# Kernel optimization log

Measured on AMD Instinct MI355X. Metric: run time of the kernel, lower is better.

The kernel has to match this reference:

```python
import jax, jax.numpy as jnp
import numpy as np

BS, N, D_IN, D_OUT = 4, 512, 64, 64
TEMP = 1.0
POOL_K = 0.5
N_KEEP = max(int(N * POOL_K), 1)  # 256
BN_EPS = 1e-5


def setup_inputs() -> dict:
    key = jax.random.key(0)
    ks = jax.random.split(key, 12)
    xav = lambda k, shape: jax.random.normal(k, shape, jnp.float32) * np.sqrt(2.0 / sum(shape))
    return {
        "x": jax.random.normal(ks[0], (BS, N, D_IN), jnp.float32),
        "att_proj_w": xav(ks[1], (D_IN, D_OUT)),
        "att_proj_b": jnp.zeros((D_OUT,), jnp.float32),
        "att_weight": xav(ks[2], (D_OUT, 1))[:, 0],  # (D_OUT,)
        "pwa_w": xav(ks[3], (D_IN, D_OUT)),
        "pwa_b": jnp.zeros((D_OUT,), jnp.float32),
        "pwoa_w": xav(ks[4], (D_IN, D_OUT)),
        "pwoa_b": jnp.zeros((D_OUT,), jnp.float32),
        "bn_gamma": jnp.ones((D_OUT,), jnp.float32),
        "bn_beta": jnp.zeros((D_OUT,), jnp.float32),
        "bn_mean": jnp.zeros((D_OUT,), jnp.float32),
        "bn_var": jnp.ones((D_OUT,), jnp.float32),
        "pool_w": xav(ks[5], (D_OUT, 1))[:, 0],  # (D_OUT,)
        "pool_b": jnp.zeros((), jnp.float32),
    }


def reference(x, att_proj_w, att_proj_b, att_weight, pwa_w, pwa_b,
              pwoa_w, pwoa_b, bn_gamma, bn_beta, bn_mean, bn_var,
              pool_w, pool_b):
    # ---- GraphAttentionLayer (eval mode: dropout off, BN uses running stats) ----
    # pairwise node product: (bs, i, j, d)
    pair = x[:, :, None, :] * x[:, None, :, :]
    a = jnp.tanh(jnp.einsum('bijd,de->bije', pair, att_proj_w) + att_proj_b)
    scores = jnp.einsum('bije,e->bij', a, att_weight) / TEMP
    att = jax.nn.softmax(scores, axis=-1)  # torch softmax over dim=-2 of (bs,i,j,1) == j axis
    agg = jnp.einsum('bij,bjd->bid', att, x)
    h = (agg @ pwa_w + pwa_b) + (x @ pwoa_w + pwoa_b)
    h = (h - bn_mean) * jax.lax.rsqrt(bn_var + BN_EPS) * bn_gamma + bn_beta
    h = jax.nn.selu(h)
    # ---- GraphPool (eval: dropout off) ----
    s = jax.nn.sigmoid(h @ pool_w + pool_b)  # (bs, N)
    _, idx = jax.lax.top_k(s, N_KEEP)        # (bs, N_KEEP), sorted desc like torch.topk
    hs = h * s[..., None]
    out = jnp.take_along_axis(hs, idx[..., None], axis=1)  # (bs, N_KEEP, D_OUT)
    return out
```

## Files before the change

### kernel.cpp

```cpp
#include <hip/hip_runtime.h>
#include <hip/hip_bf16.h>
#include <math.h>

#define BSZ 4
#define NN 512
#define DD 64
#define NKEEP 256

typedef __attribute__((ext_vector_type(8))) short short8;
typedef __attribute__((ext_vector_type(4))) float f32x4;

__device__ __forceinline__ ushort f2bf_rne(float f) {
  union { float f; unsigned u; } v; v.f = f;
  unsigned r = v.u + 0x7fffu + ((v.u >> 16) & 1u);
  return (ushort)(r >> 16);
}
__device__ __forceinline__ float bf2f(ushort h) {
  union { unsigned u; float f; } v; v.u = ((unsigned)h) << 16;
  return v.f;
}

__global__ __launch_bounds__(256, 2) void k_score(
    const float* __restrict__ x, const float* __restrict__ apw,
    const float* __restrict__ apb, const float* __restrict__ aw,
    float* __restrict__ sTp) {
  __shared__ ushort Yh[2][4 * 16 * 64];
  __shared__ ushort Yl[2][4 * 16 * 64];

  const int t = threadIdx.x;
  const int w = t >> 6, l = t & 63;
  const int bid = blockIdx.x;
  const int b = bid / 288;
  const int rem = bid % 288;
  const int eh = rem / 144;
  const int tid = rem % 144;
  int m, base;
  if (tid < 40) {
    if (tid < 4)        { m = 0; base = 0; }
    else if (tid < 12)  { m = 1; base = 4; }
    else if (tid < 24)  { m = 2; base = 12; }
    else                { m = 3; base = 24; }
  } else {
    if (tid < 60)       { m = 4; base = 40; }
    else if (tid < 84)  { m = 5; base = 60; }
    else if (tid < 112) { m = 6; base = 84; }
    else                { m = 7; base = 112; }
  }
  const int it = tid - base;
  const int i0 = it * 16;
  const int jb0 = m * 64;
  const int eh32 = eh * 32;
  const bool fast = (jb0 >= i0 + 16);

  const float* xb = x + (size_t)b * NN * DD;
  const int j0 = jb0 + w * 16;
  const bool wave_active = (j0 + 16 > i0);

  short8 ah[2], al[2];
  if (wave_active) {
    const int g = l >> 4;
    const int j = j0 + (l & 15);
    #pragma unroll
    for (int ks = 0; ks < 2; ++ks) {
      const float* xr = xb + (size_t)j * DD + ks * 32 + g * 8;
      float4 u0 = *reinterpret_cast<const float4*>(xr);
      float4 u1 = *reinterpret_cast<const float4*>(xr + 4);
      float vv[8] = {u0.x, u0.y, u0.z, u0.w, u1.x, u1.y, u1.z, u1.w};
      short8 hh, ll;
      #pragma unroll
      for (int qq = 0; qq < 8; ++qq) {
        ushort hq = f2bf_rne(vv[qq]);
        hh[qq] = (short)hq;
        ll[qq] = (short)f2bf_rne(vv[qq] - bf2f(hq));
      }
      ah[ks] = hh; al[ks] = ll;
    }
  }

  float awC = 0.f;
  #pragma unroll 8
  for (int e = 0; e < 32; ++e) awC += aw[eh32 + e];

  const int bi_g = l >> 4;
  const int bdq = (l & 15) * 4;
  auto build = [&](int rnd, int bf) {
    const int e = eh32 + rnd * 4 + w;
    float wt[4];
    #pragma unroll
    for (int k = 0; k < 4; ++k) wt[k] = apw[(bdq + k) * 64 + e];
    #pragma unroll
    for (int i2 = 0; i2 < 4; ++i2) {
      const int i = i2 * 4 + bi_g;
      float4 xv = *reinterpret_cast<const float4*>(
          xb + (size_t)(i0 + i) * DD + bdq);
      const float p0v = xv.x * wt[0], p1v = xv.y * wt[1];
      const float p2v = xv.z * wt[2], p3v = xv.w * wt[3];
      const ushort h0 = f2bf_rne(p0v), h1 = f2bf_rne(p1v);
      const ushort h2 = f2bf_rne(p2v), h3 = f2bf_rne(p3v);
      uint2 hw, lw;
      hw.x = (uint)h0 | ((uint)h1 << 16);
      hw.y = (uint)h2 | ((uint)h3 << 16);
      lw.x = (uint)f2bf_rne(p0v - bf2f(h0)) | ((uint)f2bf_rne(p1v - bf2f(h1)) << 16);
      lw.y = (uint)f2bf_rne(p2v - bf2f(h2)) | ((uint)f2bf_rne(p3v - bf2f(h3)) << 16);
      const int byteoff = (w * 2048 + (i * 64 + bdq) * 2) ^ ((i & 7) << 4);
      *reinterpret_cast<uint2*>(reinterpret_cast<char*>(Yh[bf]) + byteoff) = hw;
      *reinterpret_cast<uint2*>(reinterpret_cast<char*>(Yl[bf]) + byteoff) = lw;
    }
  };

  const int il = l & 15, g = l >> 4;
  const int fbyte0 = ((il * 64 + g * 8) * 2) ^ ((il & 7) << 4);
  const int fbyte1 = ((il * 64 + 32 + g * 8) * 2) ^ ((il & 7) << 4);
  const float K2 = 2.8853900817779268f;

  f32x4 srews = (f32x4){0.f, 0.f, 0.f, 0.f};

  build(0, 0);

  #pragma unroll 1
  for (int r = 0; r < 8; ++r) {
    __syncthreads();
    const char* Ph = reinterpret_cast<const char*>(Yh[r & 1]);
    const char* Pl = reinterpret_cast<const char*>(Yl[r & 1]);

    short8 cbh0, cbh1, cbl0, cbl1;
    if (wave_active) {
      cbh0 = *reinterpret_cast<const short8*>(Ph + fbyte0);
      cbh1 = *reinterpret_cast<const short8*>(Ph + fbyte1);
      cbl0 = *reinterpret_cast<const short8*>(Pl + fbyte0);
      cbl1 = *reinterpret_cast<const short8*>(Pl + fbyte1);
    }
    if (r < 7) build(r + 1, (r + 1) & 1);

    if (wave_active) {
      #pragma unroll
      for (int p = 0; p < 4; ++p) {
        short8 nbh0, nbh1, nbl0, nbl1;
        if (p < 3) {
          nbh0 = *reinterpret_cast<const short8*>(Ph + (p + 1) * 2048 + fbyte0);
          nbh1 = *reinterpret_cast<const short8*>(Ph + (p + 1) * 2048 + fbyte1);
          nbl0 = *reinterpret_cast<const short8*>(Pl + (p + 1) * 2048 + fbyte0);
          nbl1 = *reinterpret_cast<const short8*>(Pl + (p + 1) * 2048 + fbyte1);
        }
        f32x4 a0 = (f32x4){0.f, 0.f, 0.f, 0.f};
        f32x4 a1 = (f32x4){0.f, 0.f, 0.f, 0.f};
        a0 = __builtin_amdgcn_mfma_f32_16x16x32_bf16(ah[0], cbh0, a0, 0, 0, 0);
        a1 = __builtin_amdgcn_mfma_f32_16x16x32_bf16(ah[1], cbh1, a1, 0, 0, 0);
        a0 = __builtin_amdgcn_mfma_f32_16x16x32_bf16(ah[0], cbl0, a0, 0, 0, 0);
        a1 = __builtin_amdgcn_mfma_f32_16x16x32_bf16(ah[1], cbl1, a1, 0, 0, 0);
        a0 = __builtin_amdgcn_mfma_f32_16x16x32_bf16(al[0], cbh0, a0, 0, 0, 0);
        a1 = __builtin_amdgcn_mfma_f32_16x16x32_bf16(al[1], cbh1, a1, 0, 0, 0);

        const int e = eh32 + r * 4 + p;
        const float bias = apb[e];
        const float aw2 = 2.f * aw[e];
        #pragma unroll
        for (int rr = 0; rr < 4; ++rr) {
          const float vv = a0[rr] + a1[rr] + bias;
          const float ex = __builtin_amdgcn_exp2f(vv * K2);
          const float rc = __builtin_amdgcn_rcpf(ex + 1.0f);
          srews[rr] = fmaf(-aw2, rc, srews[rr]);
        }
        cbh0 = nbh0; cbh1 = nbh1; cbl0 = nbl0; cbl1 = nbl1;
      }
    }
  }

  f32x4 sv4;
  #pragma unroll
  for (int rr = 0; rr < 4; ++rr) sv4[rr] = srews[rr] + awC;

  float* plane = sTp + ((size_t)(eh * 4 + b)) * NN * NN;
  const int iv = i0 + il;
  if (fast) {
    #pragma unroll
    for (int rr = 0; rr < 4; ++rr)
      plane[(size_t)(j0 + g * 4 + rr) * NN + iv] = sv4[rr];
    __syncthreads();
    float* T = reinterpret_cast<float*>(Yh[0]);
    {
      const int byteoff = ((il * 64 + w * 16 + g * 4) * 4) ^ ((il & 7) << 4);
      *reinterpret_cast<f32x4*>(reinterpret_cast<char*>(T) + byteoff) = sv4;
    }
    __syncthreads();
    {
      const int row = t >> 4, cb4 = (t & 15) * 4;
      const int byteoff = ((row * 64 + cb4) * 4) ^ ((row & 7) << 4);
      f32x4 v = *reinterpret_cast<const f32x4*>(
          reinterpret_cast<const char*>(T) + byteoff);
      *reinterpret_cast<f32x4*>(plane + (size_t)(i0 + row) * NN + jb0 + cb4) = v;
    }
  } else if (wave_active) {
    #pragma unroll
    for (int rr = 0; rr < 4; ++rr) {
      const int jv = j0 + g * 4 + rr;
      if (jv >= iv) plane[(size_t)iv * NN + jv] = sv4[rr];
      if (jv > iv) plane[(size_t)jv * NN + iv] = sv4[rr];
    }
  }
}

__global__ __launch_bounds__(256) void k_soft(
    const float* __restrict__ x, const float* __restrict__ sTp,
    const float* __restrict__ pwa, const float* __restrict__ pwab,
    const float* __restrict__ pwoa, const float* __restrict__ pwob,
    const float* __restrict__ gam, const float* __restrict__ bet,
    const float* __restrict__ mu, const float* __restrict__ var,
    const float* __restrict__ poolw, const float* __restrict__ poolb,
    float* __restrict__ h, float* __restrict__ s) {
  __shared__ float ssc[2][512];
  __shared__ float srm[2][4], srs[2][4];
  __shared__ float sagg[4][2][64];
  __shared__ float rag[2][64], xis[2][64];

  const int t = threadIdx.x;
  const int w = t >> 6, l = t & 63;
  const int b = blockIdx.x >> 8;
  const int rp = blockIdx.x & 255;
  const int i_r0 = rp * 2, i_r1 = i_r0 + 1;
  const float* xb = x + (size_t)b * NN * DD;
  const float* pl0 = sTp + (size_t)b * NN * NN;
  const float* pl1 = sTp + (size_t)(4 + b) * NN * NN;
  const int jw = w * 128;

  const size_t o0 = (size_t)i_r0 * NN + jw + l;
  const size_t o1 = (size_t)i_r1 * NN + jw + l;
  float r0a = pl0[o0] + pl1[o0];
  float r0b = pl0[o0 + 64] + pl1[o0 + 64];
  float r1a = pl0[o1] + pl1[o1];
  float r1b = pl0[o1 + 64] + pl1[o1 + 64];
  float m0 = fmaxf(r0a, r0b), m1 = fmaxf(r1a, r1b);
  #pragma unroll
  for (int off = 32; off; off >>= 1) {
    m0 = fmaxf(m0, __shfl_xor(m0, off, 64));
    m1 = fmaxf(m1, __shfl_xor(m1, off, 64));
  }
  if (l == 0) { srm[0][w] = m0; srm[1][w] = m1; }
  __syncthreads();
  m0 = fmaxf(fmaxf(srm[0][0], srm[0][1]), fmaxf(srm[0][2], srm[0][3]));
  m1 = fmaxf(fmaxf(srm[1][0], srm[1][1]), fmaxf(srm[1][2], srm[1][3]));

  const float L2E = 1.4426950408889634f;
  float e0a = __builtin_amdgcn_exp2f((r0a - m0) * L2E);
  float e0b = __builtin_amdgcn_exp2f((r0b - m0) * L2E);
  float e1a = __builtin_amdgcn_exp2f((r1a - m1) * L2E);
  float e1b = __builtin_amdgcn_exp2f((r1b - m1) * L2E);
  float ps0 = e0a + e0b, ps1 = e1a + e1b;
  #pragma unroll
  for (int off = 32; off; off >>= 1) {
    ps0 += __shfl_xor(ps0, off, 64);
    ps1 += __shfl_xor(ps1, off, 64);
  }
  if (l == 0) { srs[0][w] = ps0; srs[1][w] = ps1; }
  __syncthreads();
  const float inv0 = 1.f / (srs[0][0] + srs[0][1] + srs[0][2] + srs[0][3]);
  const float inv1 = 1.f / (srs[1][0] + srs[1][1] + srs[1][2] + srs[1][3]);
  ssc[0][jw + l] = e0a * inv0;
  ssc[0][jw + 64 + l] = e0b * inv0;
  ssc[1][jw + l] = e1a * inv1;
  ssc[1][jw + 64 + l] = e1b * inv1;
  __syncthreads();

  float g0a = 0.f, g0b = 0.f, g1a = 0.f, g1b = 0.f;
  #pragma unroll 4
  for (int jj = 0; jj < 128; jj += 2) {
    const int j = jw + jj;
    const float xv0 = xb[(size_t)j * DD + l];
    const float xv1 = xb[(size_t)(j + 1) * DD + l];
    g0a = fmaf(ssc[0][j], xv0, g0a);
    g1a = fmaf(ssc[1][j], xv0, g1a);
    g0b = fmaf(ssc[0][j + 1], xv1, g0b);
    g1b = fmaf(ssc[1][j + 1], xv1, g1b);
  }
  sagg[w][0][l] = g0a + g0b;
  sagg[w][1][l] = g1a + g1b;
  __syncthreads();

  if (w < 2) {
    const int irow = i_r0 + w;
    rag[w][l] = sagg[0][w][l] + sagg[1][w][l] + sagg[2][w][l] + sagg[3][w][l];
    xis[w][l] = xb[(size_t)irow * DD + l];
    float acc = 0.f;
    #pragma unroll 8
    for (int d = 0; d < 64; ++d) {
      acc = fmaf(rag[w][d], pwa[d * 64 + l], acc);
      acc = fmaf(xis[w][d], pwoa[d * 64 + l], acc);
    }
    acc += pwab[l] + pwob[l];
    float hb = (acc - mu[l]) * rsqrtf(var[l] + 1e-5f) * gam[l] + bet[l];
    const float SC = 1.0507009873554805f, AL = 1.6732632423543772f;
    float hv = hb > 0.f ? SC * hb : SC * AL * expm1f(hb);
    h[((size_t)(b * NN + irow)) * DD + l] = hv;

    float p = hv * poolw[l];
    #pragma unroll
    for (int off = 32; off; off >>= 1) p += __shfl_xor(p, off, 64);
    if (l == 0) s[b * NN + irow] = 1.f / (1.f + expf(-(p + poolb[0])));
  }
}

__global__ __launch_bounds__(512) void k_sel(
    const float* __restrict__ s, const float* __restrict__ h,
    float* __restrict__ out) {
  __shared__ float svv[NN];
  __shared__ int inv[NKEEP];
  __shared__ float sval[NKEEP];
  const int b = blockIdx.x, t = threadIdx.x;
  svv[t] = s[b * NN + t];
  __syncthreads();

  const float my = svv[t];
  int r = 0;
  #pragma unroll 4
  for (int j0 = 0; j0 < NN; j0 += 4) {
    float4 v = *reinterpret_cast<const float4*>(&svv[j0]);
    r += (v.x > my) || (v.x == my && (j0 + 0) < t);
    r += (v.y > my) || (v.y == my && (j0 + 1) < t);
    r += (v.z > my) || (v.z == my && (j0 + 2) < t);
    r += (v.w > my) || (v.w == my && (j0 + 3) < t);
  }
  if (r < NKEEP) { inv[r] = t; sval[r] = my; }
  __syncthreads();

  #pragma unroll
  for (int pos = t; pos < NKEEP * 16; pos += 512) {
    const int kk = pos >> 4, d4 = (pos & 15) * 4;
    const int i = inv[kk];
    const float sc = sval[kk];
    float4 v = *reinterpret_cast<const float4*>(
        h + ((size_t)(b * NN + i)) * DD + d4);
    v.x *= sc; v.y *= sc; v.z *= sc; v.w *= sc;
    *reinterpret_cast<float4*>(out + ((size_t)(b * NKEEP + kk)) * DD + d4) = v;
  }
}

extern "C" void kernel_launch(void* const* d_in, const int* in_sizes, int n_in,
                              void* d_out, int out_size, void* d_ws, size_t ws_size,
                              hipStream_t stream) {
  const float* x     = (const float*)d_in[0];
  const float* apw   = (const float*)d_in[1];
  const float* apb   = (const float*)d_in[2];
  const float* aw    = (const float*)d_in[3];
  const float* pwa   = (const float*)d_in[4];
  const float* pwab  = (const float*)d_in[5];
  const float* pwoa  = (const float*)d_in[6];
  const float* pwob  = (const float*)d_in[7];
  const float* gam   = (const float*)d_in[8];
  const float* bet   = (const float*)d_in[9];
  const float* mu    = (const float*)d_in[10];
  const float* var   = (const float*)d_in[11];
  const float* poolw = (const float*)d_in[12];
  const float* poolb = (const float*)d_in[13];
  float* out = (float*)d_out;

  float* sTp = (float*)d_ws;
  float* h   = sTp + (size_t)2 * BSZ * NN * NN;
  float* s   = h + (size_t)BSZ * NN * DD;

  k_score<<<1152, 256, 0, stream>>>(x, apw, apb, aw, sTp);
  k_soft<<<BSZ * 256, 256, 0, stream>>>(x, sTp, pwa, pwab, pwoa, pwob,
                                        gam, bet, mu, var, poolw, poolb, h, s);
  k_sel<<<BSZ, 512, 0, stream>>>(s, h, out);
}
```

Measured before the change: 71.26 us.

## Restructure score kernel: pair-product A operand, pre-split weights, single score plane

The score kernel now forms the elementwise pair product x_i*x_j as the MFMA A operand and multiplies by a pre-split (hi/lo bf16) transposed weight matrix held in registers, covering all 64 output features per block. The previous version used a two-half-plane layout that k_soft had to sum. A new prep kernel builds the split weights and a triangular tile table, and k_score runs as 64-thread single-wave blocks over 16x16 upper-triangle tiles. Each tile writes its transposed mirror through a small shared tile. This drops the per-round shared-memory staging and syncs, and halves the score-plane traffic. In exchange it adds an extra kernel launch, more MFMAs per output element, and per-row cross-lane shuffle reductions.

```diff
diff --git a/kernel.cpp b/kernel.cpp
--- a/kernel.cpp
+++ b/kernel.cpp
@@ -19,189 +19,171 @@
   union { unsigned u; float f; } v; v.u = ((unsigned)h) << 16;
   return v.f;
 }
-
-__global__ __launch_bounds__(256, 2) void k_score(
-    const float* __restrict__ x, const float* __restrict__ apw,
-    const float* __restrict__ apb, const float* __restrict__ aw,
-    float* __restrict__ sTp) {
-  __shared__ ushort Yh[2][4 * 16 * 64];
-  __shared__ ushort Yl[2][4 * 16 * 64];
-
-  const int t = threadIdx.x;
-  const int w = t >> 6, l = t & 63;
-  const int bid = blockIdx.x;
-  const int b = bid / 288;
-  const int rem = bid % 288;
-  const int eh = rem / 144;
-  const int tid = rem % 144;
-  int m, base;
-  if (tid < 40) {
-    if (tid < 4)        { m = 0; base = 0; }
-    else if (tid < 12)  { m = 1; base = 4; }
-    else if (tid < 24)  { m = 2; base = 12; }
-    else                { m = 3; base = 24; }
-  } else {
-    if (tid < 60)       { m = 4; base = 40; }
-    else if (tid < 84)  { m = 5; base = 60; }
-    else if (tid < 112) { m = 6; base = 84; }
-    else                { m = 7; base = 112; }
-  }
-  const int it = tid - base;
-  const int i0 = it * 16;
-  const int jb0 = m * 64;
-  const int eh32 = eh * 32;
-  const bool fast = (jb0 >= i0 + 16);
+__device__ __forceinline__ void split2(float a, float b, uint& hu, uint& lu) {
+  const ushort ha = f2bf_rne(a), hb = f2bf_rne(b);
+  hu = (uint)ha | ((uint)hb << 16);
+  const ushort la = f2bf_rne(a - bf2f(ha));
+  const ushort lb = f2bf_rne(b - bf2f(hb));
+  lu = (uint)la | ((uint)lb << 16);
+}
+
+__global__ void k_prep(const float* __restrict__ apw,
+                       ushort* __restrict__ wht, ushort* __restrict__ wlt,
+                       int* __restrict__ tile_tab) {
+  const int idx = blockIdx.x * 256 + threadIdx.x;
+  const int d = idx >> 6, e = idx & 63;
+  const float wv = apw[idx];
+  const ushort h = f2bf_rne(wv);
+  const ushort lo = f2bf_rne(wv - bf2f(h));
+  wht[e * 64 + d] = h;
+  wlt[e * 64 + d] = lo;
+  if (idx < 528) {
+    int it = 0;
+    #pragma unroll
+    for (int r = 1; r < 32; ++r) it += ((r * (65 - r)) / 2 <= idx);
+    const int jt = it + (idx - (it * (65 - it)) / 2);
+    tile_tab[idx] = it | (jt << 8);
+  }
+}
+
+__global__ __launch_bounds__(64) void k_score(
+    const float* __restrict__ x, const ushort* __restrict__ wht,
+    const ushort* __restrict__ wlt, const float* __restrict__ apb,
+    const float* __restrict__ aw, const int* __restrict__ tile_tab,
+    float* __restrict__ sT) {
+  __shared__ __align__(16) float T[16][16];
+
+  const int l = threadIdx.x;
+  const int il = l & 15, g = l >> 4;
+  const int gid = blockIdx.x;
+  const int b = gid / 528;
+  const int pid = gid - b * 528;
+  const int pk = tile_tab[pid];
+  const int it = pk & 0xff, jt = pk >> 8;
+  const int i0 = it * 16, j0 = jt * 16;
+  const bool diag = (it == jt);
 
   const float* xb = x + (size_t)b * NN * DD;
-  const int j0 = jb0 + w * 16;
-  const bool wave_active = (j0 + 16 > i0);
-
-  short8 ah[2], al[2];
-  if (wave_active) {
-    const int g = l >> 4;
-    const int j = j0 + (l & 15);
+  float* plane = sT + (size_t)b * NN * NN;
+
+  short8 wfh[4][2], wfl[4][2];
+  #pragma unroll
+  for (int eq = 0; eq < 4; ++eq)
     #pragma unroll
     for (int ks = 0; ks < 2; ++ks) {
-      const float* xr = xb + (size_t)j * DD + ks * 32 + g * 8;
-      float4 u0 = *reinterpret_cast<const float4*>(xr);
-      float4 u1 = *reinterpret_cast<const float4*>(xr + 4);
-      float vv[8] = {u0.x, u0.y, u0.z, u0.w, u1.x, u1.y, u1.z, u1.w};
-      short8 hh, ll;
+      const int off = (eq * 16 + il) * 64 + ks * 32 + g * 8;
+      wfh[eq][ks] = *reinterpret_cast<const short8*>(wht + off);
+      wfl[eq][ks] = *reinterpret_cast<const short8*>(wlt + off);
+    }
+
+  const float K2 = 2.8853900817779268f;
+  float aw2_4[4], bK2[4], awq = 0.f;
+  #pragma unroll
+  for (int eq = 0; eq < 4; ++eq) {
+    const float a = aw[eq * 16 + il];
+    aw2_4[eq] = 2.f * a;
+    bK2[eq] = apb[eq * 16 + il] * K2;
+    awq += a;
+  }
+  awq += __shfl_xor(awq, 1, 64);
+  awq += __shfl_xor(awq, 2, 64);
+  awq += __shfl_xor(awq, 4, 64);
+  awq += __shfl_xor(awq, 8, 64);
+  const float awC = awq;
+
+  const float* xjr = xb + (size_t)(j0 + il) * DD;
+  const float4 xj0 = *reinterpret_cast<const float4*>(xjr + g * 8);
+  const float4 xj1 = *reinterpret_cast<const float4*>(xjr + g * 8 + 4);
+  const float4 xj2 = *reinterpret_cast<const float4*>(xjr + 32 + g * 8);
+  const float4 xj3 = *reinterpret_cast<const float4*>(xjr + 32 + g * 8 + 4);
+
+  #pragma unroll 2
+  for (int ii = 0; ii < 16; ++ii) {
+    const int i_glob = i0 + ii;
+    const float* xir = xb + (size_t)i_glob * DD;
+    const float4 xi0 = *reinterpret_cast<const float4*>(xir + g * 8);
+    const float4 xi1 = *reinterpret_cast<const float4*>(xir + g * 8 + 4);
+    const float4 xi2 = *reinterpret_cast<const float4*>(xir + 32 + g * 8);
+    const float4 xi3 = *reinterpret_cast<const float4*>(xir + 32 + g * 8 + 4);
+
+    union { uint u[4]; short8 s; } hA, lA, hB, lB;
+    split2(xj0.x * xi0.x, xj0.y * xi0.y, hA.u[0], lA.u[0]);
+    split2(xj0.z * xi0.z, xj0.w * xi0.w, hA.u[1], lA.u[1]);
+    split2(xj1.x * xi1.x, xj1.y * xi1.y, hA.u[2], lA.u[2]);
+    split2(xj1.z * xi1.z, xj1.w * xi1.w, hA.u[3], lA.u[3]);
+    split2(xj2.x * xi2.x, xj2.y * xi2.y, hB.u[0], lB.u[0]);
+    split2(xj2.z * xi2.z, xj2.w * xi2.w, hB.u[1], lB.u[1]);
+    split2(xj3.x * xi3.x, xj3.y * xi3.y, hB.u[2], lB.u[2]);
+    split2(xj3.z * xi3.z, xj3.w * xi3.w, hB.u[3], lB.u[3]);
+
+    f32x4 acc[4];
+    #pragma unroll
+    for (int eq = 0; eq < 4; ++eq) acc[eq] = (f32x4){0.f, 0.f, 0.f, 0.f};
+    #pragma unroll
+    for (int eq = 0; eq < 4; ++eq) {
+      acc[eq] = __builtin_amdgcn_mfma_f32_16x16x32_bf16(hA.s, wfh[eq][0], acc[eq], 0, 0, 0);
+      acc[eq] = __builtin_amdgcn_mfma_f32_16x16x32_bf16(hA.s, wfl[eq][0], acc[eq], 0, 0, 0);
+      acc[eq] = __builtin_amdgcn_mfma_f32_16x16x32_bf16(lA.s, wfh[eq][0], acc[eq], 0, 0, 0);
+      acc[eq] = __builtin_amdgcn_mfma_f32_16x16x32_bf16(hB.s, wfh[eq][1], acc[eq], 0, 0, 0);
+      acc[eq] = __builtin_amdgcn_mfma_f32_16x16x32_bf16(hB.s, wfl[eq][1], acc[eq], 0, 0, 0);
+      acc[eq] = __builtin_amdgcn_mfma_f32_16x16x32_bf16(lB.s, wfh[eq][1], acc[eq], 0, 0, 0);
+    }
+
+    float neg[4] = {0.f, 0.f, 0.f, 0.f};
+    #pragma unroll
+    for (int eq = 0; eq < 4; ++eq)
       #pragma unroll
-      for (int qq = 0; qq < 8; ++qq) {
-        ushort hq = f2bf_rne(vv[qq]);
-        hh[qq] = (short)hq;
-        ll[qq] = (short)f2bf_rne(vv[qq] - bf2f(hq));
+      for (int rr = 0; rr < 4; ++rr) {
+        const float ex = __builtin_amdgcn_exp2f(fmaf(acc[eq][rr], K2, bK2[eq]));
+        const float rc = __builtin_amdgcn_rcpf(ex + 1.0f);
+        neg[rr] = fmaf(aw2_4[eq], rc, neg[rr]);
       }
-      ah[ks] = hh; al[ks] = ll;
-    }
-  }
-
-  float awC = 0.f;
-  #pragma unroll 8
-  for (int e = 0; e < 32; ++e) awC += aw[eh32 + e];
-
-  const int bi_g = l >> 4;
-  const int bdq = (l & 15) * 4;
-  auto build = [&](int rnd, int bf) {
-    const int e = eh32 + rnd * 4 + w;
-    float wt[4];
-    #pragma unroll
-    for (int k = 0; k < 4; ++k) wt[k] = apw[(bdq + k) * 64 + e];
-    #pragma unroll
-    for (int i2 = 0; i2 < 4; ++i2) {
-      const int i = i2 * 4 + bi_g;
-      float4 xv = *reinterpret_cast<const float4*>(
-          xb + (size_t)(i0 + i) * DD + bdq);
-      const float p0v = xv.x * wt[0], p1v = xv.y * wt[1];
-      const float p2v = xv.z * wt[2], p3v = xv.w * wt[3];
-      const ushort h0 = f2bf_rne(p0v), h1 = f2bf_rne(p1v);
-      const ushort h2 = f2bf_rne(p2v), h3 = f2bf_rne(p3v);
-      uint2 hw, lw;
-      hw.x = (uint)h0 | ((uint)h1 << 16);
-      hw.y = (uint)h2 | ((uint)h3 << 16);
-      lw.x = (uint)f2bf_rne(p0v - bf2f(h0)) | ((uint)f2bf_rne(p1v - bf2f(h1)) << 16);
-      lw.y = (uint)f2bf_rne(p2v - bf2f(h2)) | ((uint)f2bf_rne(p3v - bf2f(h3)) << 16);
-      const int byteoff = (w * 2048 + (i * 64 + bdq) * 2) ^ ((i & 7) << 4);
-      *reinterpret_cast<uint2*>(reinterpret_cast<char*>(Yh[bf]) + byteoff) = hw;
-      *reinterpret_cast<uint2*>(reinterpret_cast<char*>(Yl[bf]) + byteoff) = lw;
-    }
-  };
-
-  const int il = l & 15, g = l >> 4;
-  const int fbyte0 = ((il * 64 + g * 8) * 2) ^ ((il & 7) << 4);
-  const int fbyte1 = ((il * 64 + 32 + g * 8) * 2) ^ ((il & 7) << 4);
-  const float K2 = 2.8853900817779268f;
-
-  f32x4 srews = (f32x4){0.f, 0.f, 0.f, 0.f};
-
-  build(0, 0);
-
-  #pragma unroll 1
-  for (int r = 0; r < 8; ++r) {
-    __syncthreads();
-    const char* Ph = reinterpret_cast<const char*>(Yh[r & 1]);
-    const char* Pl = reinterpret_cast<const char*>(Yl[r & 1]);
-
-    short8 cbh0, cbh1, cbl0, cbl1;
-    if (wave_active) {
-      cbh0 = *reinterpret_cast<const short8*>(Ph + fbyte0);
-      cbh1 = *reinterpret_cast<const short8*>(Ph + fbyte1);
-      cbl0 = *reinterpret_cast<const short8*>(Pl + fbyte0);
-      cbl1 = *reinterpret_cast<const short8*>(Pl + fbyte1);
-    }
-    if (r < 7) build(r + 1, (r + 1) & 1);
-
-    if (wave_active) {
-      #pragma unroll
-      for (int p = 0; p < 4; ++p) {
-        short8 nbh0, nbh1, nbl0, nbl1;
-        if (p < 3) {
-          nbh0 = *reinterpret_cast<const short8*>(Ph + (p + 1) * 2048 + fbyte0);
-          nbh1 = *reinterpret_cast<const short8*>(Ph + (p + 1) * 2048 + fbyte1);
-          nbl0 = *reinterpret_cast<const short8*>(Pl + (p + 1) * 2048 + fbyte0);
-          nbl1 = *reinterpret_cast<const short8*>(Pl + (p + 1) * 2048 + fbyte1);
-        }
-        f32x4 a0 = (f32x4){0.f, 0.f, 0.f, 0.f};
-        f32x4 a1 = (f32x4){0.f, 0.f, 0.f, 0.f};
-        a0 = __builtin_amdgcn_mfma_f32_16x16x32_bf16(ah[0], cbh0, a0, 0, 0, 0);
-        a1 = __builtin_amdgcn_mfma_f32_16x16x32_bf16(ah[1], cbh1, a1, 0, 0, 0);
-        a0 = __builtin_amdgcn_mfma_f32_16x16x32_bf16(ah[0], cbl0, a0, 0, 0, 0);
-        a1 = __builtin_amdgcn_mfma_f32_16x16x32_bf16(ah[1], cbl1, a1, 0, 0, 0);
-        a0 = __builtin_amdgcn_mfma_f32_16x16x32_bf16(al[0], cbh0, a0, 0, 0, 0);
-        a1 = __builtin_amdgcn_mfma_f32_16x16x32_bf16(al[1], cbh1, a1, 0, 0, 0);
-
-        const int e = eh32 + r * 4 + p;
-        const float bias = apb[e];
-        const float aw2 = 2.f * aw[e];
+    #pragma unroll
+    for (int rr = 0; rr < 4; ++rr) {
+      neg[rr] += __shfl_xor(neg[rr], 1, 64);
+      neg[rr] += __shfl_xor(neg[rr], 2, 64);
+      neg[rr] += __shfl_xor(neg[rr], 4, 64);
+      neg[rr] += __shfl_xor(neg[rr], 8, 64);
+    }
+    const f32x4 sc = {awC - neg[0], awC - neg[1], awC - neg[2], awC - neg[3]};
+
+    if (il == 0) {
+      if (!diag) {
+        *reinterpret_cast<f32x4*>(plane + (size_t)i_glob * NN + j0 + g * 4) = sc;
+      } else {
         #pragma unroll
         for (int rr = 0; rr < 4; ++rr) {
-          const float vv = a0[rr] + a1[rr] + bias;
-          const float ex = __builtin_amdgcn_exp2f(vv * K2);
-          const float rc = __builtin_amdgcn_rcpf(ex + 1.0f);
-          srews[rr] = fmaf(-aw2, rc, srews[rr]);
+          const int jv = j0 + g * 4 + rr;
+          if (jv >= i_glob) plane[(size_t)i_glob * NN + jv] = sc[rr];
         }
-        cbh0 = nbh0; cbh1 = nbh1; cbl0 = nbl0; cbl1 = nbl1;
       }
-    }
-  }
-
-  f32x4 sv4;
-  #pragma unroll
-  for (int rr = 0; rr < 4; ++rr) sv4[rr] = srews[rr] + awC;
-
-  float* plane = sTp + ((size_t)(eh * 4 + b)) * NN * NN;
-  const int iv = i0 + il;
-  if (fast) {
-    #pragma unroll
-    for (int rr = 0; rr < 4; ++rr)
-      plane[(size_t)(j0 + g * 4 + rr) * NN + iv] = sv4[rr];
-    __syncthreads();
-    float* T = reinterpret_cast<float*>(Yh[0]);
-    {
-      const int byteoff = ((il * 64 + w * 16 + g * 4) * 4) ^ ((il & 7) << 4);
-      *reinterpret_cast<f32x4*>(reinterpret_cast<char*>(T) + byteoff) = sv4;
-    }
-    __syncthreads();
-    {
-      const int row = t >> 4, cb4 = (t & 15) * 4;
-      const int byteoff = ((row * 64 + cb4) * 4) ^ ((row & 7) << 4);
-      f32x4 v = *reinterpret_cast<const f32x4*>(
-          reinterpret_cast<const char*>(T) + byteoff);
-      *reinterpret_cast<f32x4*>(plane + (size_t)(i0 + row) * NN + jb0 + cb4) = v;
-    }
-  } else if (wave_active) {
-    #pragma unroll
-    for (int rr = 0; rr < 4; ++rr) {
-      const int jv = j0 + g * 4 + rr;
-      if (jv >= iv) plane[(size_t)iv * NN + jv] = sv4[rr];
-      if (jv > iv) plane[(size_t)jv * NN + iv] = sv4[rr];
+      *reinterpret_cast<f32x4*>(&T[ii][g * 4]) = sc;
+    }
+  }
+
+  __syncthreads();
+
+  {
+    const int jv = il;
+    const float m0 = T[g * 4 + 0][jv];
+    const float m1 = T[g * 4 + 1][jv];
+    const float m2 = T[g * 4 + 2][jv];
+    const float m3 = T[g * 4 + 3][jv];
+    if (!diag) {
+      const f32x4 mv = {m0, m1, m2, m3};
+      *reinterpret_cast<f32x4*>(plane + (size_t)(j0 + jv) * NN + i0 + g * 4) = mv;
+    } else {
+      const int jr = j0 + jv;
+      if (jr > i0 + g * 4 + 0) plane[(size_t)jr * NN + i0 + g * 4 + 0] = m0;
+      if (jr > i0 + g * 4 + 1) plane[(size_t)jr * NN + i0 + g * 4 + 1] = m1;
+      if (jr > i0 + g * 4 + 2) plane[(size_t)jr * NN + i0 + g * 4 + 2] = m2;
+      if (jr > i0 + g * 4 + 3) plane[(size_t)jr * NN + i0 + g * 4 + 3] = m3;
     }
   }
 }
 
 __global__ __launch_bounds__(256) void k_soft(
-    const float* __restrict__ x, const float* __restrict__ sTp,
+    const float* __restrict__ x, const float* __restrict__ sT,
     const float* __restrict__ pwa, const float* __restrict__ pwab,
     const float* __restrict__ pwoa, const float* __restrict__ pwob,
     const float* __restrict__ gam, const float* __restrict__ bet,
@@ -219,16 +201,15 @@
   const int rp = blockIdx.x & 255;
   const int i_r0 = rp * 2, i_r1 = i_r0 + 1;
   const float* xb = x + (size_t)b * NN * DD;
-  const float* pl0 = sTp + (size_t)b * NN * NN;
-  const float* pl1 = sTp + (size_t)(4 + b) * NN * NN;
+  const float* pl0 = sT + (size_t)b * NN * NN;
   const int jw = w * 128;
 
   const size_t o0 = (size_t)i_r0 * NN + jw + l;
   const size_t o1 = (size_t)i_r1 * NN + jw + l;
-  float r0a = pl0[o0] + pl1[o0];
-  float r0b = pl0[o0 + 64] + pl1[o0 + 64];
-  float r1a = pl0[o1] + pl1[o1];
-  float r1b = pl0[o1 + 64] + pl1[o1 + 64];
+  float r0a = pl0[o0];
+  float r0b = pl0[o0 + 64];
+  float r1a = pl0[o1];
+  float r1b = pl0[o1 + 64];
   float m0 = fmaxf(r0a, r0b), m1 = fmaxf(r1a, r1b);
   #pragma unroll
   for (int off = 32; off; off >>= 1) {
@@ -353,12 +334,16 @@
   const float* poolb = (const float*)d_in[13];
   float* out = (float*)d_out;
 
-  float* sTp = (float*)d_ws;
-  float* h   = sTp + (size_t)2 * BSZ * NN * NN;
-  float* s   = h + (size_t)BSZ * NN * DD;
-
-  k_score<<<1152, 256, 0, stream>>>(x, apw, apb, aw, sTp);
-  k_soft<<<BSZ * 256, 256, 0, stream>>>(x, sTp, pwa, pwab, pwoa, pwob,
+  float* sT    = (float*)d_ws;
+  float* h     = sT + (size_t)BSZ * NN * NN;
+  float* s     = h + (size_t)BSZ * NN * DD;
+  ushort* wht  = (ushort*)(s + BSZ * NN);
+  ushort* wlt  = wht + 4096;
+  int* tile_tab = (int*)(wlt + 4096);
+
+  k_prep<<<16, 256, 0, stream>>>(apw, wht, wlt, tile_tab);
+  k_score<<<2112, 64, 0, stream>>>(x, wht, wlt, apb, aw, tile_tab, sT);
+  k_soft<<<BSZ * 256, 256, 0, stream>>>(x, sT, pwa, pwab, pwoa, pwob,
                                         gam, bet, mu, var, poolw, poolb, h, s);
   k_sel<<<BSZ, 512, 0, stream>>>(s, h, out);
 }
```

Result: slower. 76.65 us (+7.6%).
